# Kernel tuning notes

Hardware: AMD Instinct MI355X
Metric: run time of the kernel (lower is better)

The kernel has to match this reference:

```python
import jax, jax.numpy as jnp
import numpy as np
import math

EMBED_DIM = 1024
NUM_HEADS = 16
HEAD_DIM = EMBED_DIM // NUM_HEADS
B, S = 2, 2048


def setup_inputs() -> dict:
    key = jax.random.key(0)
    ks = jax.random.split(key, 13)
    sc = 1.0 / math.sqrt(EMBED_DIM)
    inp = {
        "query": jax.random.normal(ks[0], (B, S, EMBED_DIM), jnp.float32),
        "key": jax.random.normal(ks[1], (B, S, EMBED_DIM), jnp.float32),
        "value": jax.random.normal(ks[2], (B, S, EMBED_DIM), jnp.float32),
        "input_patch_mask": jax.random.randint(ks[3], (B, S), 0, 2, jnp.int32),
        "Wq": jax.random.normal(ks[4], (EMBED_DIM, EMBED_DIM), jnp.float32) * sc,
        "bq": jnp.zeros((EMBED_DIM,), jnp.float32),
        "Wk": jax.random.normal(ks[5], (EMBED_DIM, EMBED_DIM), jnp.float32) * sc,
        "bk": jnp.zeros((EMBED_DIM,), jnp.float32),
        "Wv": jax.random.normal(ks[6], (EMBED_DIM, EMBED_DIM), jnp.float32) * sc,
        "bv": jnp.zeros((EMBED_DIM,), jnp.float32),
        "Wo": jax.random.normal(ks[7], (EMBED_DIM, EMBED_DIM), jnp.float32) * sc,
        "bo": jnp.zeros((EMBED_DIM,), jnp.float32),
    }
    return inp


def _masked_softmax(scores, mask):
    # Equivalent to masked_fill(-inf) -> softmax -> nan_to_num(0.0):
    # fully-masked rows produce exactly 0, without generating NaNs.
    neg_inf = jnp.array(-jnp.inf, scores.dtype)
    s = jnp.where(mask, scores, neg_inf)
    m = jnp.max(s, axis=-1, keepdims=True)
    m_safe = jnp.where(jnp.isfinite(m), m, jnp.zeros_like(m))
    e = jnp.where(mask, jnp.exp(s - m_safe), 0.0)
    denom = jnp.sum(e, axis=-1, keepdims=True)
    denom = jnp.where(denom == 0.0, 1.0, denom)
    return e / denom


def reference(query, key, value, input_patch_mask, Wq, bq, Wk, bk, Wv, bv, Wo, bo):
    b, s, d = query.shape
    h, hd = NUM_HEADS, HEAD_DIM
    q = (query @ Wq.T + bq).reshape(b, s, h, hd).transpose(0, 2, 1, 3)  # [b,h,s,hd]
    k = (key @ Wk.T + bk).reshape(b, s, h, hd).transpose(0, 2, 1, 3)
    v = (value @ Wv.T + bv).reshape(b, s, h, hd).transpose(0, 2, 1, 3)
    scores = jnp.einsum("bhqd,bhkd->bhqk", q, k) / math.sqrt(hd)
    # mask[b,i,j] = patch_mask[b,i] * patch_mask[b,j]
    mask = (input_patch_mask[:, :, None] * input_patch_mask[:, None, :]) > 0
    attn = _masked_softmax(scores, mask[:, None, :, :])  # dropout in eval mode = identity
    context = jnp.einsum("bhqk,bhkd->bhqd", attn, v)
    context = context.transpose(0, 2, 1, 3).reshape(b, s, d)
    return context @ Wo.T + bo
```

## Files before the change

kernel.cpp:

```cpp
#include <hip/hip_runtime.h>
#include <cstdint>
#include <cstddef>

#define EMBED 1024
#define NHEAD 16
#define HD    64
#define BATCH 2
#define SEQ   2048
#define MROWS (BATCH*SEQ)
#define QSCALE 0.1803368801111137f

typedef __bf16 bf16;
typedef __bf16 bf16x8 __attribute__((ext_vector_type(8)));
typedef float  f32x4  __attribute__((ext_vector_type(4)));
typedef unsigned int u32;

#if __has_builtin(__builtin_amdgcn_exp2f)
#define EXP2(x) __builtin_amdgcn_exp2f(x)
#else
#define EXP2(x) exp2f(x)
#endif

typedef const u32 __attribute__((address_space(1)))* gp_t;
typedef u32 __attribute__((address_space(3)))* lp_t;

__device__ __forceinline__ void g2l16(const void* g, void* l) {
  __builtin_amdgcn_global_load_lds((gp_t)(uintptr_t)g, (lp_t)(u32)(uintptr_t)l, 16, 0, 0);
}

#define MFMA(a, b, c) __builtin_amdgcn_mfma_f32_16x16x32_bf16((a), (b), (c), 0, 0, 0)

#define SZX8 ((MROWS*EMBED)/8)
#define SZW8 ((EMBED*EMBED)/8)

__global__ void cast_all(const float* __restrict__ q, const float* __restrict__ k,
                         const float* __restrict__ v, const float* __restrict__ wq,
                         const float* __restrict__ wk, const float* __restrict__ wv,
                         const float* __restrict__ wo,
                         bf16* xq, bf16* xk, bf16* xv,
                         bf16* wqb, bf16* wkb, bf16* wvb, bf16* wob) {
  int z = blockIdx.y;
  const float* in; bf16* out;
  switch (z) {
    case 0: in = q;  out = xq;  break;
    case 1: in = k;  out = xk;  break;
    case 2: in = v;  out = xv;  break;
    case 3: in = wq; out = wqb; break;
    case 4: in = wk; out = wkb; break;
    case 5: in = wv; out = wvb; break;
    default: in = wo; out = wob; break;
  }
  int n8 = (z < 3) ? SZX8 : SZW8;
  int i = blockIdx.x * blockDim.x + threadIdx.x;
  if (i >= n8) return;
  const float4* p = (const float4*)in;
  float4 a = p[2*i], b = p[2*i+1];
  union { bf16 h[8]; uint4 u; } r;
  r.h[0] = (bf16)a.x; r.h[1] = (bf16)a.y; r.h[2] = (bf16)a.z; r.h[3] = (bf16)a.w;
  r.h[4] = (bf16)b.x; r.h[5] = (bf16)b.y; r.h[6] = (bf16)b.z; r.h[7] = (bf16)b.w;
  ((uint4*)out)[i] = r.u;
}

#define BM 128
#define BN 128
#define BK 32
#define NKI (EMBED/BK)

__device__ __forceinline__ void gemm_core(
    const bf16* __restrict__ A, const bf16* __restrict__ W,
    int m0, int n0, bf16* Al, bf16* Bl, f32x4 (&acc)[4][4])
{
  const int tid  = threadIdx.x;
  const int lane = tid & 63, wid = tid >> 6;
  const int quad = lane >> 4, l16 = lane & 15;
  const int wm = wid >> 1, wn = wid & 1;

  const int R = tid >> 2, Cc = tid & 3;
  const int gcol = (Cc ^ ((R >> 1) & 3)) * 8;
  const bf16* Ag = A + (size_t)(m0 + R) * EMBED + gcol;
  const bf16* Bg = W + (size_t)(n0 + R) * EMBED + gcol;
  bf16* AlW = Al + wid * 512;
  bf16* BlW = Bl + wid * 512;

#define GSTAGE(ki) do { \
    const int nb_ = (ki) % 3; const int k0_ = (ki) * BK; \
    g2l16(Ag + k0_,                    AlW + nb_*4096); \
    g2l16(Ag + (size_t)64*EMBED + k0_, AlW + nb_*4096 + 2048); \
    g2l16(Bg + k0_,                    BlW + nb_*4096); \
    g2l16(Bg + (size_t)64*EMBED + k0_, BlW + nb_*4096 + 2048); } while (0)

  GSTAGE(0);
  GSTAGE(1);

  for (int ki = 0; ki < NKI; ++ki) {
    if (ki < NKI - 1) asm volatile("s_waitcnt vmcnt(4)" ::: "memory");
    else              asm volatile("s_waitcnt vmcnt(0)" ::: "memory");
    __builtin_amdgcn_s_barrier();
    __builtin_amdgcn_sched_barrier(0);
    if (ki + 2 < NKI) GSTAGE(ki + 2);

    const bf16* Ac = Al + (ki % 3)*4096;
    const bf16* Bc = Bl + (ki % 3)*4096;
    bf16x8 af[4], bg[4];
#pragma unroll
    for (int i = 0; i < 4; ++i) {
      int ra = wm*64 + i*16 + l16;
      af[i] = *(const bf16x8*)(Ac + ra*32 + ((quad ^ ((ra>>1)&3))*8));
      int rb = wn*64 + i*16 + l16;
      bg[i] = *(const bf16x8*)(Bc + rb*32 + ((quad ^ ((rb>>1)&3))*8));
    }
#pragma unroll
    for (int i = 0; i < 4; ++i)
#pragma unroll
      for (int j = 0; j < 4; ++j)
        acc[i][j] = MFMA(af[i], bg[j], acc[i][j]);
  }
#undef GSTAGE
}

__global__ __launch_bounds__(256) void qkv_kernel(
    const bf16* __restrict__ Xq, const bf16* __restrict__ Xk, const bf16* __restrict__ Xv,
    const bf16* __restrict__ Wq, const bf16* __restrict__ Wk, const bf16* __restrict__ Wv,
    const float* __restrict__ bq, const float* __restrict__ bk, const float* __restrict__ bv,
    bf16* __restrict__ Qp, bf16* __restrict__ Kp, bf16* __restrict__ VTg)
{
  __shared__ bf16 Al[3*BM*BK];
  __shared__ bf16 Bl[3*BN*BK];

  const unsigned hw = blockIdx.x + 8u*blockIdx.y + 256u*blockIdx.z;
  const unsigned wk = (hw & 7u)*96u + (hw >> 3);
  const int z  = (int)(wk >> 8);
  const unsigned rem = wk & 255u;
  const int by = (int)(rem >> 3), bx = (int)(rem & 7u);

  const bf16* A = z==0 ? Xq : z==1 ? Xk : Wv;
  const bf16* W = z==0 ? Wq : z==1 ? Wk : Xv;
  const float* bias = z==0 ? bq : z==1 ? bk : bv;
  const float scale = (z==0) ? QSCALE : 1.0f;
  const int m0 = (z < 2) ? by * BM : bx * BM;
  const int n0 = (z < 2) ? bx * BN : by * BN;

  f32x4 acc[4][4] = {};
  gemm_core(A, W, m0, n0, Al, Bl, acc);

  const int lane = threadIdx.x & 63, wid = threadIdx.x >> 6;
  const int quad = lane >> 4, l16 = lane & 15;
  const int wm = wid >> 1, wn = wid & 1;

  if (z < 2) {
#pragma unroll
    for (int i = 0; i < 4; ++i) {
#pragma unroll
      for (int j = 0; j < 4; ++j) {
        int col = n0 + wn*64 + j*16 + l16;
        float bv2 = bias[col];
        bf16* outp = (z == 0) ? Qp : Kp;
#pragma unroll
        for (int r = 0; r < 4; ++r) {
          int row = m0 + wm*64 + i*16 + quad*4 + r;
          outp[(size_t)row*EMBED + col] = (bf16)((acc[i][j][r] + bv2) * scale);
        }
      }
    }
  } else {
    const int tcol0 = n0 + wn*64;
    const int bb   = tcol0 >> 11;
    const int tile = (tcol0 & (SEQ-1)) >> 6;
    const int pbase = (l16 >> 2)*8 + (l16 & 3)*2;
#pragma unroll
    for (int i = 0; i < 4; ++i) {
      float4 bv4 = *(const float4*)&bias[m0 + wm*64 + i*16 + quad*4];
#pragma unroll
      for (int r = 0; r < 4; ++r) {
        int e = m0 + wm*64 + i*16 + quad*4 + r;
        int hh = e >> 6, dd = e & (HD-1);
        float bvr = (r==0) ? bv4.x : (r==1) ? bv4.y : (r==2) ? bv4.z : bv4.w;
        union { bf16 h[2]; u32 u; } p01, p23;
        p01.h[0] = (bf16)(acc[i][0][r] + bvr);
        p01.h[1] = (bf16)(acc[i][1][r] + bvr);
        p23.h[0] = (bf16)(acc[i][2][r] + bvr);
        p23.h[1] = (bf16)(acc[i][3][r] + bvr);
        size_t base = (((size_t)bb*NHEAD + hh)*HD + dd)*SEQ + tile*64;
        *(u32*)&VTg[base + pbase]      = p01.u;
        *(u32*)&VTg[base + 32 + pbase] = p23.u;
      }
    }
  }
}

__global__ __launch_bounds__(256) void oproj_kernel(
    const bf16* __restrict__ Ctx, const bf16* __restrict__ Wo,
    const float* __restrict__ bo, float* __restrict__ out)
{
  __shared__ bf16 Al[3*128*32];
  __shared__ bf16 Bl[3*64*32];
  const int tid  = threadIdx.x;
  const int lane = tid & 63, wid = tid >> 6;
  const int quad = lane >> 4, l16 = lane & 15;

  const unsigned hw = blockIdx.x + 16u*blockIdx.y;
  const unsigned wk = (hw & 7u)*64u + (hw >> 3);
  const int m0 = (int)(wk >> 4) * 128, n0 = (int)(wk & 15u) * 64;

  const int R = tid >> 2, Cc = tid & 3;
  const int gcol = (Cc ^ ((R >> 1) & 3)) * 8;
  const bf16* Ag = Ctx + (size_t)(m0 + R) * EMBED + gcol;
  const bf16* Bg = Wo  + (size_t)(n0 + R) * EMBED + gcol;
  bf16* AlW = Al + wid * 512;
  bf16* BlW = Bl + wid * 512;

#define OSTAGE(ki) do { \
    const int nb_ = (ki) % 3; const int k0_ = (ki) * BK; \
    g2l16(Ag + k0_,                    AlW + nb_*4096); \
    g2l16(Ag + (size_t)64*EMBED + k0_, AlW + nb_*4096 + 2048); \
    g2l16(Bg + k0_,                    BlW + nb_*2048); } while (0)

  OSTAGE(0);
  OSTAGE(1);

  f32x4 acc[2][4] = {};
  for (int ki = 0; ki < NKI; ++ki) {
    if (ki < NKI - 1) asm volatile("s_waitcnt vmcnt(3)" ::: "memory");
    else              asm volatile("s_waitcnt vmcnt(0)" ::: "memory");
    __builtin_amdgcn_s_barrier();
    __builtin_amdgcn_sched_barrier(0);
    if (ki + 2 < NKI) OSTAGE(ki + 2);

    const bf16* Ac = Al + (ki % 3)*4096;
    const bf16* Bc = Bl + (ki % 3)*2048;
    bf16x8 af[2], bg[4];
#pragma unroll
    for (int u = 0; u < 2; ++u) {
      int ra = wid*32 + u*16 + l16;
      af[u] = *(const bf16x8*)(Ac + ra*32 + ((quad ^ ((ra>>1)&3))*8));
    }
#pragma unroll
    for (int j = 0; j < 4; ++j) {
      int rb = j*16 + l16;
      bg[j] = *(const bf16x8*)(Bc + rb*32 + ((quad ^ ((rb>>1)&3))*8));
    }
#pragma unroll
    for (int u = 0; u < 2; ++u)
#pragma unroll
      for (int j = 0; j < 4; ++j)
        acc[u][j] = MFMA(af[u], bg[j], acc[u][j]);
  }
#undef OSTAGE

#pragma unroll
  for (int u = 0; u < 2; ++u)
#pragma unroll
    for (int j = 0; j < 4; ++j) {
      int col = n0 + j*16 + l16;
      float bv = bo[col];
#pragma unroll
      for (int r = 0; r < 4; ++r) {
        int row = m0 + wid*32 + u*16 + quad*4 + r;
        out[(size_t)row*EMBED + col] = (acc[u][j][r] + bv);
      }
    }
}

#define NT  (SEQ/64)

__global__ __launch_bounds__(512, 2) void attn_kernel(
    const bf16* __restrict__ Qp, const bf16* __restrict__ Kp, const bf16* __restrict__ VT,
    const int* __restrict__ pmask, bf16* __restrict__ Ctx)
{
  __shared__ __align__(16) bf16 SM[5*4096];

  const int qt = blockIdx.x, h = blockIdx.y, b = blockIdx.z;
  const int tid = threadIdx.x, lane = tid & 63, wid = tid >> 6;
  const int quad = lane >> 4, l16 = lane & 15;
  const int w4 = wid & 3, h2 = wid >> 2;
  const int qrow0 = qt*128 + w4*32;

  bf16x8 qf[2][2];
#pragma unroll
  for (int qg = 0; qg < 2; ++qg) {
    const size_t qoff = (size_t)(b*SEQ + qrow0 + qg*16 + l16)*EMBED + h*HD;
    qf[qg][0] = *(const bf16x8*)(Qp + qoff + quad*8);
    qf[qg][1] = *(const bf16x8*)(Qp + qoff + 32 + quad*8);
  }

  bf16 onev = (bf16)1.0f;
  bf16x8 ones = {onev, onev, onev, onev, onev, onev, onev, onev};

  const bf16* Kg  = Kp + (size_t)b*SEQ*EMBED + h*HD;
  const bf16* VTg = VT + (size_t)(b*NHEAD + h)*HD*SEQ;
  const int*  kmw = pmask + b*SEQ + h2*32 + quad*4;

  const int R = tid >> 3;
  const int Cc = tid & 7;
  const int scol = (Cc ^ (R & 7)) * 8;

  f32x4 o[2][4] = {};
  f32x4 lacc[2] = {};
  bf16x8 pa[2] = {};

#define STAGE_K(kt, buf) g2l16(Kg + (size_t)((kt)*64 + R)*EMBED + scol, SM + (buf)*4096 + wid*512)
#define STAGE_V(kt, buf) g2l16(VTg + (size_t)R*SEQ + (kt)*64 + scol,    SM + 8192 + (buf)*4096 + wid*512)

  int4 kq0 = *(const int4*)(kmw);
  int4 kq1 = *(const int4*)(kmw + 16);
  STAGE_K(0, 0);
  STAGE_V(0, 0);

  for (int kt = 0; kt < NT; ++kt) {
    asm volatile("s_waitcnt vmcnt(0)" ::: "memory");
    __builtin_amdgcn_s_barrier();
    __builtin_amdgcn_sched_barrier(0);

    float fm0[4], fm1[4];
    fm0[0] = (float)kq0.x; fm0[1] = (float)kq0.y; fm0[2] = (float)kq0.z; fm0[3] = (float)kq0.w;
    fm1[0] = (float)kq1.x; fm1[1] = (float)kq1.y; fm1[2] = (float)kq1.z; fm1[3] = (float)kq1.w;
    __builtin_amdgcn_sched_barrier(0);

    if (kt + 1 < NT) {
      kq0 = *(const int4*)(kmw + (kt+1)*64);
      kq1 = *(const int4*)(kmw + (kt+1)*64 + 16);
      STAGE_K(kt + 1, (kt + 1) & 1);
      STAGE_V(kt + 1, (kt + 1) % 3);
    }

    if (kt > 0) {
      const bf16* Vc = SM + 8192 + ((kt - 1) % 3)*4096;
      lacc[0] = MFMA(pa[0], ones, lacc[0]);
      lacc[1] = MFMA(pa[1], ones, lacc[1]);
#pragma unroll
      for (int t = 0; t < 4; ++t) {
        int rd = t*16 + l16, sd = rd & 7;
        bf16x8 vf = *(const bf16x8*)(Vc + rd*64 + (((h2*4 + quad) ^ sd)*8));
        o[0][t] = MFMA(pa[0], vf, o[0][t]);
        o[1][t] = MFMA(pa[1], vf, o[1][t]);
      }
    }

    const bf16* Kc = SM + (kt & 1)*4096;
#pragma unroll
    for (int kg = 0; kg < 2; ++kg) {
      int ra = h2*32 + kg*16 + l16, sa = ra & 7;
      bf16x8 kfa = *(const bf16x8*)(Kc + ra*64 + ((quad       ^ sa)*8));
      bf16x8 kfb = *(const bf16x8*)(Kc + ra*64 + (((quad + 4) ^ sa)*8));
      const float* fm = kg ? fm1 : fm0;
#pragma unroll
      for (int qg = 0; qg < 2; ++qg) {
        f32x4 s = {};
        s = MFMA(kfa, qf[qg][0], s);
        s = MFMA(kfb, qf[qg][1], s);
        pa[qg][0 + kg] = (bf16)(EXP2(s[0]) * fm[0]);
        pa[qg][2 + kg] = (bf16)(EXP2(s[1]) * fm[1]);
        pa[qg][4 + kg] = (bf16)(EXP2(s[2]) * fm[2]);
        pa[qg][6 + kg] = (bf16)(EXP2(s[3]) * fm[3]);
      }
    }
  }

  {
    const bf16* Vc = SM + 8192 + ((NT - 1) % 3)*4096;
    lacc[0] = MFMA(pa[0], ones, lacc[0]);
    lacc[1] = MFMA(pa[1], ones, lacc[1]);
#pragma unroll
    for (int t = 0; t < 4; ++t) {
      int rd = t*16 + l16, sd = rd & 7;
      bf16x8 vf = *(const bf16x8*)(Vc + rd*64 + (((h2*4 + quad) ^ sd)*8));
      o[0][t] = MFMA(pa[0], vf, o[0][t]);
      o[1][t] = MFMA(pa[1], vf, o[1][t]);
    }
  }

  __syncthreads();
  f32x4* rp = (f32x4*)SM;
  const int idx = w4*64 + lane;
  if (h2 == 1) {
#pragma unroll
    for (int qg = 0; qg < 2; ++qg) {
#pragma unroll
      for (int t = 0; t < 4; ++t) rp[(qg*4 + t)*256 + idx] = o[qg][t];
      rp[2048 + qg*256 + idx] = lacc[qg];
    }
  }
  __syncthreads();
  if (h2 == 0) {
#pragma unroll
    for (int qg = 0; qg < 2; ++qg) {
      lacc[qg] += rp[2048 + qg*256 + idx];
#pragma unroll
      for (int t = 0; t < 4; ++t) o[qg][t] += rp[(qg*4 + t)*256 + idx];
    }
#pragma unroll
    for (int qg = 0; qg < 2; ++qg) {
      int4 qm = *(const int4*)(pmask + b*SEQ + qrow0 + qg*16 + quad*4);
      float inv[4];
      inv[0] = (qm.x && lacc[qg][0] > 0.f) ? 1.0f / lacc[qg][0] : 0.0f;
      inv[1] = (qm.y && lacc[qg][1] > 0.f) ? 1.0f / lacc[qg][1] : 0.0f;
      inv[2] = (qm.z && lacc[qg][2] > 0.f) ? 1.0f / lacc[qg][2] : 0.0f;
      inv[3] = (qm.w && lacc[qg][3] > 0.f) ? 1.0f / lacc[qg][3] : 0.0f;
#pragma unroll
      for (int t = 0; t < 4; ++t)
#pragma unroll
        for (int r = 0; r < 4; ++r) {
          int row = b*SEQ + qrow0 + qg*16 + quad*4 + r;
          Ctx[(size_t)row*EMBED + h*HD + t*16 + l16] = (bf16)(o[qg][t][r] * inv[r]);
        }
    }
  }
}

extern "C" void kernel_launch(void* const* d_in, const int* in_sizes, int n_in,
                              void* d_out, int out_size, void* d_ws, size_t ws_size,
                              hipStream_t stream)
{
  const float* query = (const float*)d_in[0];
  const float* key   = (const float*)d_in[1];
  const float* value = (const float*)d_in[2];
  const int*   pm    = (const int*)d_in[3];
  const float* Wq = (const float*)d_in[4];
  const float* bq = (const float*)d_in[5];
  const float* Wk = (const float*)d_in[6];
  const float* bk = (const float*)d_in[7];
  const float* Wv = (const float*)d_in[8];
  const float* bv = (const float*)d_in[9];
  const float* Wo = (const float*)d_in[10];
  const float* bo = (const float*)d_in[11];
  float* out = (float*)d_out;

  const size_t SZ_X = (size_t)MROWS * EMBED;
  const size_t SZ_W = (size_t)EMBED * EMBED;

  bf16* p   = (bf16*)d_ws;
  bf16* Xq  = p; p += SZ_X;
  bf16* Xk  = p; p += SZ_X;
  bf16* Xv  = p; p += SZ_X;
  bf16* Wqb = p; p += SZ_W;
  bf16* Wkb = p; p += SZ_W;
  bf16* Wvb = p; p += SZ_W;
  bf16* Wob = p; p += SZ_W;
  bf16* Qp  = p; p += SZ_X;
  bf16* Kp  = p; p += SZ_X;
  bf16* VTg = p; p += SZ_X;
  bf16* Ctx = p; p += SZ_X;

  dim3 gc((unsigned)(SZX8/256), 7);
  cast_all<<<gc, 256, 0, stream>>>(query, key, value, Wq, Wk, Wv, Wo,
                                   Xq, Xk, Xv, Wqb, Wkb, Wvb, Wob);

  dim3 gq(EMBED/BN, MROWS/BM, 3);
  qkv_kernel<<<gq, 256, 0, stream>>>(Xq, Xk, Xv, Wqb, Wkb, Wvb, bq, bk, bv, Qp, Kp, VTg);

  dim3 ga(SEQ/128, NHEAD, BATCH);
  attn_kernel<<<ga, 512, 0, stream>>>(Qp, Kp, VTg, pm, Ctx);

  dim3 gg(EMBED/64, MROWS/128);
  oproj_kernel<<<gg, 256, 0, stream>>>(Ctx, Wob, bo, out);
}
```

Measured before the change: 216.3 us.

## Deepen attention K/V prefetch to two tiles ahead with partial vmcnt waits

Grows the LDS staging to triple-buffered K and quad-buffered V so global-to-LDS loads are issued two key tiles ahead instead of one. The per-iteration wait changes from a full vmcnt(0) drain to a partial vmcnt wait, so the next tile's loads can stay in flight during compute. It also raises wave priority around the PV MFMA block. The larger LDS footprint (56KB per block) may limit occupancy, and the vmcnt counts assume an exact number of outstanding loads per stage.

```diff
diff --git a/kernel.cpp b/kernel.cpp
--- a/kernel.cpp
+++ b/kernel.cpp
@@ -267,7 +267,7 @@
     const bf16* __restrict__ Qp, const bf16* __restrict__ Kp, const bf16* __restrict__ VT,
     const int* __restrict__ pmask, bf16* __restrict__ Ctx)
 {
-  __shared__ __align__(16) bf16 SM[5*4096];
+  __shared__ __align__(16) bf16 SM[7*4096];
 
   const int qt = blockIdx.x, h = blockIdx.y, b = blockIdx.z;
   const int tid = threadIdx.x, lane = tid & 63, wid = tid >> 6;
@@ -298,33 +298,40 @@
   f32x4 lacc[2] = {};
   bf16x8 pa[2] = {};
 
-#define STAGE_K(kt, buf) g2l16(Kg + (size_t)((kt)*64 + R)*EMBED + scol, SM + (buf)*4096 + wid*512)
-#define STAGE_V(kt, buf) g2l16(VTg + (size_t)R*SEQ + (kt)*64 + scol,    SM + 8192 + (buf)*4096 + wid*512)
-
+#define STAGE_K(kt) g2l16(Kg + (size_t)((kt)*64 + R)*EMBED + scol, SM + ((kt)%3)*4096 + wid*512)
+#define STAGE_V(kt) g2l16(VTg + (size_t)R*SEQ + (kt)*64 + scol,    SM + (3 + ((kt)&3))*4096 + wid*512)
+
+  STAGE_K(0); STAGE_V(0);
+  __builtin_amdgcn_sched_barrier(0);
   int4 kq0 = *(const int4*)(kmw);
   int4 kq1 = *(const int4*)(kmw + 16);
-  STAGE_K(0, 0);
-  STAGE_V(0, 0);
+  __builtin_amdgcn_sched_barrier(0);
+  STAGE_K(1); STAGE_V(1);
+  __builtin_amdgcn_sched_barrier(0);
 
   for (int kt = 0; kt < NT; ++kt) {
-    asm volatile("s_waitcnt vmcnt(0)" ::: "memory");
+    if (kt < NT - 1) asm volatile("s_waitcnt vmcnt(4)" ::: "memory");
+    else             asm volatile("s_waitcnt vmcnt(2)" ::: "memory");
     __builtin_amdgcn_s_barrier();
+    __builtin_amdgcn_sched_barrier(0);
+
+    int4 kqn0 = kq0, kqn1 = kq1;
+    if (kt + 1 < NT) {
+      kqn0 = *(const int4*)(kmw + (kt+1)*64);
+      kqn1 = *(const int4*)(kmw + (kt+1)*64 + 16);
+    }
+    __builtin_amdgcn_sched_barrier(0);
+    if (kt + 2 < NT) { STAGE_K(kt + 2); STAGE_V(kt + 2); }
     __builtin_amdgcn_sched_barrier(0);
 
     float fm0[4], fm1[4];
     fm0[0] = (float)kq0.x; fm0[1] = (float)kq0.y; fm0[2] = (float)kq0.z; fm0[3] = (float)kq0.w;
     fm1[0] = (float)kq1.x; fm1[1] = (float)kq1.y; fm1[2] = (float)kq1.z; fm1[3] = (float)kq1.w;
-    __builtin_amdgcn_sched_barrier(0);
-
-    if (kt + 1 < NT) {
-      kq0 = *(const int4*)(kmw + (kt+1)*64);
-      kq1 = *(const int4*)(kmw + (kt+1)*64 + 16);
-      STAGE_K(kt + 1, (kt + 1) & 1);
-      STAGE_V(kt + 1, (kt + 1) % 3);
-    }
+    kq0 = kqn0; kq1 = kqn1;
 
     if (kt > 0) {
-      const bf16* Vc = SM + 8192 + ((kt - 1) % 3)*4096;
+      const bf16* Vc = SM + (3 + ((kt - 1) & 3))*4096;
+      __builtin_amdgcn_s_setprio(1);
       lacc[0] = MFMA(pa[0], ones, lacc[0]);
       lacc[1] = MFMA(pa[1], ones, lacc[1]);
 #pragma unroll
@@ -334,9 +341,10 @@
         o[0][t] = MFMA(pa[0], vf, o[0][t]);
         o[1][t] = MFMA(pa[1], vf, o[1][t]);
       }
-    }
-
-    const bf16* Kc = SM + (kt & 1)*4096;
+      __builtin_amdgcn_s_setprio(0);
+    }
+
+    const bf16* Kc = SM + (kt % 3)*4096;
 #pragma unroll
     for (int kg = 0; kg < 2; ++kg) {
       int ra = h2*32 + kg*16 + l16, sa = ra & 7;
@@ -357,7 +365,7 @@
   }
 
   {
-    const bf16* Vc = SM + 8192 + ((NT - 1) % 3)*4096;
+    const bf16* Vc = SM + (3 + ((NT - 1) & 3))*4096;
     lacc[0] = MFMA(pa[0], ones, lacc[0]);
     lacc[1] = MFMA(pa[1], ones, lacc[1]);
 #pragma unroll
```

Measured after the change: 222.9 us. 3.1% more time.
